# Performance work log

Hardware: AMD Instinct MI355X
Metric: run time of the kernel (lower is better)

The kernel has to match this reference:

```python
import jax, jax.numpy as jnp
import numpy as np

EDGE = 32          # ImageEdge
KPOOL = 16         # pool_kernel_size = ImageEdge // 2
POOLED = 17        # 1 + ImageEdge - pool_kernel_size
NH = 12            # num_attention_heads
HD = 64            # head_dim
HID = 768          # hidden_size
SR = 2             # ScaleRatio


def setup_inputs() -> dict:
    key = jax.random.key(0)
    k1, k2, k3, k4 = jax.random.split(key, 4)
    B, Q = 8, 2048
    return {
        "image_hidden_states": jax.random.normal(k1, (B, EDGE * EDGE, HID), jnp.float32),
        "text_hidden_states": jax.random.normal(k2, (B, Q, HID), jnp.float32),
        "W_in": jax.random.normal(k3, (HID, HID), jnp.float32) * 0.02,   # input_proj (no bias)
        "W_up": jax.random.normal(k4, (HD, HD * SR * SR), jnp.float32) * 0.02,  # up_proj (no bias)
    }


def reference(image_hidden_states, text_hidden_states, W_in, W_up):
    img, txt = image_hidden_states, text_hidden_states
    B, S, HSZ = img.shape            # S = 1024
    Q = txt.shape[1]
    residual = img

    # cross-attention: text queries attend over image keys
    q = txt.reshape(B, Q, NH, HD).transpose(0, 2, 1, 3)   # [B,H,Q,D]
    k = img.reshape(B, S, NH, HD).transpose(0, 2, 1, 3)   # [B,H,S,D]
    attn = jnp.einsum('bhqd,bhkd->bhqk', q, k) / jnp.sqrt(jnp.float32(HD))
    attn = jax.nn.softmax(attn, axis=-1)                  # [B,H,Q,S]
    # dropout is identity in eval mode

    # pooled attention saliency map
    image_attn = attn.sum(axis=2).reshape(B, NH, EDGE, EDGE)
    pooled = jax.lax.reduce_window(
        image_attn, 0.0, jax.lax.add,
        window_dimensions=(1, 1, KPOOL, KPOOL),
        window_strides=(1, 1, 1, 1), padding='VALID') / (KPOOL * KPOOL)   # [B,H,17,17]
    idx = jnp.argmax(pooled.reshape(B, NH, -1), axis=-1)  # [B,H]
    row = (idx // POOLED).reshape(-1)
    col = (idx % POOLED).reshape(-1)

    # gather the argmax-selected 16x16 region per (batch, head)
    states = img.reshape(B, S, NH, HD).transpose(0, 2, 1, 3)
    states = states.reshape(B * NH, EDGE, EDGE, HD)
    slice_one = lambda s, r, c: jax.lax.dynamic_slice(s, (r, c, 0), (KPOOL, KPOOL, HD))
    region = jax.vmap(slice_one)(states, row, col)        # [B*H,16,16,D]

    # pixel-shuffle upsample back to 32x32
    up = region @ W_up                                    # [B*H,16,16,4*D]
    up = up.reshape(B, NH, KPOOL, KPOOL, SR, SR, HD)
    up = up.transpose(0, 1, 2, 4, 3, 5, 6)                # [B,H,16,2,16,2,D]
    up = up.reshape(B, NH, EDGE * EDGE, HD)
    out = up.transpose(0, 2, 1, 3).reshape(B, EDGE * EDGE, HSZ)

    # dense proj + gelu + residual
    out = jax.nn.gelu(out @ W_in, approximate=False)
    return residual + out
```

## Files before the change

### kernel.cpp

```cpp
#include <hip/hip_runtime.h>
#include <cstdint>
#include <cstddef>

#define BB    8
#define NH    12
#define BH    96
#define SS    1024
#define QQ    2048
#define DD    64
#define HID   768
#define EDGE  32
#define KPOOL 16
#define POOLED 17

typedef short bf16x8 __attribute__((ext_vector_type(8)));
typedef _Float16 f16x8 __attribute__((ext_vector_type(8)));
typedef float f32x4  __attribute__((ext_vector_type(4)));

#define MFMA16B(a, b, c) __builtin_amdgcn_mfma_f32_16x16x32_bf16((a), (b), (c), 0, 0, 0)
#define MFMA16H(a, b, c) __builtin_amdgcn_mfma_f32_16x16x32_f16((a), (b), (c), 0, 0, 0)

#define QSCALE 0.18033688011112042f

#if __has_builtin(__builtin_amdgcn_exp2f)
#define EXP2(x) __builtin_amdgcn_exp2f(x)
#else
#define EXP2(x) exp2f(x)
#endif

__device__ __forceinline__ short f2bf(float x) {
    unsigned u = __builtin_bit_cast(unsigned, x);
    u = u + 0x7fffu + ((u >> 16) & 1u);
    return (short)(u >> 16);
}
__device__ __forceinline__ short f2h(float x) {
    _Float16 h = (_Float16)x;
    return __builtin_bit_cast(short, h);
}
__device__ __forceinline__ f16x8 ash(bf16x8 v) {
    return __builtin_bit_cast(f16x8, v);
}

__device__ __forceinline__ size_t fragaddr(int row, int k) {
    return ((size_t)(row >> 4) * 24 + (k >> 5)) * 512 + ((k >> 3) & 3) * 128
         + (row & 15) * 8 + (k & 7);
}


__global__ __launch_bounds__(256) void k_castq(const float* __restrict__ txt,
                                               short* __restrict__ Qs) {
    int i = blockIdx.x * 256 + threadIdx.x;
    int quad = i & 3, kh = (i >> 2) & 1;
    int row = i >> 3;
    int c = row & 15, g = row >> 4;
    int q = row & 2047, bh = row >> 11;
    int b = bh / NH, h = bh - b * NH;
    const float* sp = txt + ((size_t)b * QQ + q) * HID + h * DD + kh * 32 + quad * 8;
    bf16x8 vh, vl;
#pragma unroll
    for (int j = 0; j < 8; j++) {
        float x = sp[j] * QSCALE;
        _Float16 hi = (_Float16)x;
        vh[j] = __builtin_bit_cast(short, hi);
        vl[j] = f2h(x - (float)hi);
    }
    short* dp = Qs + (size_t)g * 2048 + kh * 512 + quad * 128 + c * 8;
    *(bf16x8*)dp = vh;
    *(bf16x8*)(dp + 1024) = vl;
}

__global__ __launch_bounds__(256) void k_castk(const float* __restrict__ img,
                                               short* __restrict__ Ks) {
    int i = blockIdx.x * 256 + threadIdx.x;
    int quad = i & 3, kh = (i >> 2) & 1;
    int row = i >> 3;
    int c = row & 15, g = row >> 4;
    int s = row & 1023, bh = row >> 10;
    int b = bh / NH, h = bh - b * NH;
    const float* sp = img + ((size_t)b * SS + s) * HID + h * DD + kh * 32 + quad * 8;
    bf16x8 vh;
#pragma unroll
    for (int j = 0; j < 8; j++) {
        float x = sp[j];
        _Float16 hi = (_Float16)x;
        vh[j] = __builtin_bit_cast(short, hi);
    }
    short* dp = Ks + (size_t)g * 2048 + kh * 512 + quad * 128 + c * 8;
    *(bf16x8*)dp = vh;
}

__global__ __launch_bounds__(256) void k_castw(const float* __restrict__ W,
                                               const float* __restrict__ Wup,
                                               short* __restrict__ Wt,
                                               short* __restrict__ Wupb) {
    if (blockIdx.x == 144) {
        for (int i = threadIdx.x; i < 16384; i += 256) {
            int k = i >> 8, n = i & 255;
            int addr = (n >> 4) * 1024 + (k >> 5) * 512 + ((k >> 3) & 3) * 128
                     + (n & 15) * 8 + (k & 7);
            Wupb[addr] = f2bf(Wup[k * 256 + n]);
        }
        return;
    }
    __shared__ float T[64][65];
    int bx = blockIdx.x % 12, by = blockIdx.x / 12;
    for (int i = threadIdx.x; i < 4096; i += 256) {
        int r = i >> 6, cc = i & 63;
        T[r][cc] = W[(size_t)(by * 64 + r) * HID + bx * 64 + cc];
    }
    __syncthreads();
    for (int i = threadIdx.x; i < 4096; i += 256) {
        int r = i >> 6, cc = i & 63;
        int n = bx * 64 + r, k = by * 64 + cc;
        Wt[fragaddr(n, k)] = f2bf(T[cc][r]);
    }
}

__global__ __launch_bounds__(256, 2) void k_lsum(const short* __restrict__ Qs,
                                                 const short* __restrict__ Ks,
                                                 float* __restrict__ Lsum) {
    __shared__ short Kt[2][4096];
    int bh = blockIdx.x % BH;
    int qblk = blockIdx.x / BH;
    int tid = threadIdx.x;
    int w = tid >> 6, lane = tid & 63;
    int quad = lane >> 4, c = lane & 15;

    f16x8 a0[4], a1[4];
    const short* qbase = Qs + (size_t)bh * QQ * 128;
#pragma unroll
    for (int t = 0; t < 4; t++) {
        const short* ap = qbase + (size_t)(qblk * 16 + w * 4 + t) * 2048 + lane * 8;
        a0[t] = ash(*(const bf16x8*)(ap));
        a1[t] = ash(*(const bf16x8*)(ap + 512));
    }
    f32x4 lacc[4];
#pragma unroll
    for (int t = 0; t < 4; t++) lacc[t] = (f32x4){0.f, 0.f, 0.f, 0.f};

    const short* kbase = Ks + (size_t)bh * SS * 128;
    int sg = tid >> 7, so = tid & 127;
    bf16x8 st[2];
#pragma unroll
    for (int j = 0; j < 2; j++)
        st[j] = *(const bf16x8*)(kbase + (size_t)(j * 2 + sg) * 2048 + so * 8);

    for (int t1 = 0; t1 < 16; t1++) {
        int buf = t1 & 1;
#pragma unroll
        for (int j = 0; j < 2; j++)
            *(bf16x8*)(&Kt[buf][j * 2048 + tid * 8]) = st[j];
        if (t1 + 1 < 16) {
#pragma unroll
            for (int j = 0; j < 2; j++)
                st[j] = *(const bf16x8*)(kbase + (size_t)((t1 + 1) * 4 + j * 2 + sg) * 2048 + so * 8);
        }
        __syncthreads();
#pragma unroll
        for (int g = 0; g < 4; g++) {
            const short* kp = &Kt[buf][g * 1024 + lane * 8];
            f16x8 kb0 = ash(*(const bf16x8*)(kp));
            f16x8 kb1 = ash(*(const bf16x8*)(kp + 512));
#pragma unroll
            for (int t = 0; t < 4; t++) {
                f32x4 acc = (f32x4){0.f, 0.f, 0.f, 0.f};
                acc = MFMA16H(a0[t], kb0, acc);
                acc = MFMA16H(a1[t], kb1, acc);
#pragma unroll
                for (int r = 0; r < 4; r++) lacc[t][r] += EXP2(acc[r]);
            }
        }
    }
#pragma unroll
    for (int t = 0; t < 4; t++) {
#pragma unroll
        for (int r = 0; r < 4; r++) {
            float v = lacc[t][r];
            v += __shfl_xor(v, 1);
            v += __shfl_xor(v, 2);
            v += __shfl_xor(v, 4);
            v += __shfl_xor(v, 8);
            if (c == 0)
                Lsum[(size_t)bh * QQ + qblk * 256 + w * 64 + t * 16 + quad * 4 + r] = v;
        }
    }
}

__global__ __launch_bounds__(256, 2) void k_attnacc(const short* __restrict__ Qs,
                                                    const short* __restrict__ Ks,
                                                    const float* __restrict__ Lsum,
                                                    float* __restrict__ iattn) {
    __shared__ short Qt[2][8192];
    int bh = blockIdx.x % BH;
    int rem = blockIdx.x / BH;
    int sblk = rem >> 1, qh = rem & 1;
    int tid = threadIdx.x;
    int w = tid >> 6, lane = tid & 63;
    int quad = lane >> 4, c = lane & 15;

    f16x8 ah0[4], ah1[4];
    const short* kbase = Ks + (size_t)bh * SS * 128;
#pragma unroll
    for (int t = 0; t < 4; t++) {
        const short* ap = kbase + (size_t)(sblk * 16 + w * 4 + t) * 2048 + lane * 8;
        ah0[t] = ash(*(const bf16x8*)(ap));
        ah1[t] = ash(*(const bf16x8*)(ap + 512));
    }
    f32x4 racc[4];
#pragma unroll
    for (int t = 0; t < 4; t++) racc[t] = (f32x4){0.f, 0.f, 0.f, 0.f};

    const short* qbase = Qs + ((size_t)bh * QQ + qh * 1024) * 128;
    const float* lbase = Lsum + (size_t)bh * QQ + qh * 1024;

    bf16x8 st[4];
#pragma unroll
    for (int j = 0; j < 4; j++)
        st[j] = *(const bf16x8*)(qbase + (size_t)j * 2048 + tid * 8);

    for (int t2 = 0; t2 < 16; t2++) {
        int buf = t2 & 1;
#pragma unroll
        for (int j = 0; j < 4; j++)
            *(bf16x8*)(&Qt[buf][j * 2048 + tid * 8]) = st[j];
        if (t2 + 1 < 16) {
#pragma unroll
            for (int j = 0; j < 4; j++)
                st[j] = *(const bf16x8*)(qbase + (size_t)(t2 + 1) * 8192 + j * 2048 + tid * 8);
        }
        __syncthreads();
        float rl[4];
#pragma unroll
        for (int g = 0; g < 4; g++)
            rl[g] = __builtin_amdgcn_rcpf(lbase[t2 * 64 + g * 16 + c]);
#pragma unroll
        for (int g = 0; g < 4; g++) {
            const short* qp = &Qt[buf][g * 2048 + lane * 8];
            f16x8 qb0 = ash(*(const bf16x8*)(qp));
            f16x8 qb1 = ash(*(const bf16x8*)(qp + 512));
            f16x8 qb2 = ash(*(const bf16x8*)(qp + 1024));
            f16x8 qb3 = ash(*(const bf16x8*)(qp + 1536));
#pragma unroll
            for (int t = 0; t < 4; t++) {
                f32x4 acc = (f32x4){0.f, 0.f, 0.f, 0.f};
                acc = MFMA16H(ah0[t], qb0, acc);
                acc = MFMA16H(ah1[t], qb1, acc);
                acc = MFMA16H(ah0[t], qb2, acc);
                acc = MFMA16H(ah1[t], qb3, acc);
#pragma unroll
                for (int r = 0; r < 4; r++)
                    racc[t][r] = fmaf(EXP2(acc[r]), rl[g], racc[t][r]);
            }
        }
    }
#pragma unroll
    for (int t = 0; t < 4; t++) {
#pragma unroll
        for (int r = 0; r < 4; r++) {
            float v = racc[t][r];
            v += __shfl_xor(v, 1);
            v += __shfl_xor(v, 2);
            v += __shfl_xor(v, 4);
            v += __shfl_xor(v, 8);
            if (c == 0)
                atomicAdd(&iattn[(size_t)bh * SS + sblk * 256 + w * 64 + t * 16 + quad * 4 + r], v);
        }
    }
}

__global__ __launch_bounds__(256, 2) void k_up(const float* __restrict__ img,
                                               const float* __restrict__ iattn,
                                               const short* __restrict__ Wupb,
                                               short* __restrict__ Xb) {
    __shared__ short Reg[16384];
    float* F = (float*)Reg;
    float* Apool = F;
    float* Vp = F + 1024;
    float* bvp = F + 1568;
    int*   bip = (int*)(F + 1824);

    int bh = blockIdx.x >> 2, nq = blockIdx.x & 3;
    int b = bh / NH, h = bh - b * NH;
    int tid = threadIdx.x;
    int w = tid >> 6, lane = tid & 63;
    int quad = lane >> 4, c = lane & 15;

    for (int i = tid; i < 1024; i += 256) Apool[i] = iattn[(size_t)bh * SS + i];
    __syncthreads();
    for (int i = tid; i < POOLED * EDGE; i += 256) {
        int r = i >> 5, cc = i & 31;
        float s = 0.f;
#pragma unroll
        for (int k = 0; k < KPOOL; k++) s += Apool[(r + k) * EDGE + cc];
        Vp[i] = s;
    }
    __syncthreads();
    float best = -1e30f;
    int bidx = 1 << 30;
    for (int i = tid; i < POOLED * POOLED; i += 256) {
        int r = i / POOLED, cc = i - r * POOLED;
        float s = 0.f;
#pragma unroll
        for (int k = 0; k < KPOOL; k++) s += Vp[r * EDGE + cc + k];
        if (s > best || (s == best && i < bidx)) { best = s; bidx = i; }
    }
    bvp[tid] = best;
    bip[tid] = bidx;
    __syncthreads();
    for (int off = 128; off; off >>= 1) {
        if (tid < off) {
            float ov = bvp[tid + off];
            int oi = bip[tid + off];
            if (ov > bvp[tid] || (ov == bvp[tid] && oi < bip[tid])) {
                bvp[tid] = ov;
                bip[tid] = oi;
            }
        }
        __syncthreads();
    }
    int widx = bip[0];
    __syncthreads();
    int r0 = widx / POOLED, c0 = widx - r0 * POOLED;

    for (int p = tid; p < 2048; p += 256) {
        int pos = p >> 3, sub = p & 7;
        int gi = r0 + (pos >> 4), gj = c0 + (pos & 15);
        const float* sp = img + ((size_t)b * SS + gi * EDGE + gj) * HID + h * DD + sub * 8;
        bf16x8 v;
#pragma unroll
        for (int j = 0; j < 8; j++) v[j] = f2bf(sp[j]);
        *(bf16x8*)(&Reg[(pos >> 4) * 1024 + (sub >> 2) * 512 + (sub & 3) * 128 + (pos & 15) * 8]) = v;
    }
    __syncthreads();

    bf16x8 bu[4][2];
#pragma unroll
    for (int u = 0; u < 4; u++) {
#pragma unroll
        for (int kh = 0; kh < 2; kh++)
            bu[u][kh] = *(const bf16x8*)(Wupb + (nq * 4 + u) * 1024 + kh * 512 + lane * 8);
    }

#pragma unroll
    for (int t = 0; t < 4; t++) {
        int g = w * 4 + t;
        bf16x8 a0 = *(const bf16x8*)(&Reg[g * 1024 + lane * 8]);
        bf16x8 a1 = *(const bf16x8*)(&Reg[g * 1024 + 512 + lane * 8]);
#pragma unroll
        for (int u = 0; u < 4; u++) {
            f32x4 acc = (f32x4){0.f, 0.f, 0.f, 0.f};
            acc = MFMA16B(a0, bu[u][0], acc);
            acc = MFMA16B(a1, bu[u][1], acc);
#pragma unroll
            for (int r = 0; r < 4; r++) {
                int pos = g * 16 + quad * 4 + r;
                int oc = nq * 64 + u * 16 + c;
                int i16 = pos >> 4, j16 = pos & 15;
                int a = oc >> 7, bbit = (oc >> 6) & 1, dp = oc & 63;
                int p2 = (2 * i16 + a) * EDGE + (2 * j16 + bbit);
                int row = b * SS + p2, kdim = h * DD + dp;
                Xb[fragaddr(row, kdim)] = f2bf(acc[r]);
            }
        }
    }
}

__global__ __launch_bounds__(256) void k_out(const short* __restrict__ Xb,
                                             const short* __restrict__ Wt,
                                             const float* __restrict__ img,
                                             float* __restrict__ out) {
    __shared__ short At[2][4096];
    __shared__ short Bt[2][2048];
    int mblk = blockIdx.x & 63, nblk = blockIdx.x >> 6;
    int tid = threadIdx.x;
    int w = tid >> 6, lane = tid & 63;
    int quad = lane >> 4, c = lane & 15;
    int gm0 = mblk * 8, gn0 = nblk * 4;
    int m0 = mblk * 128, n0 = nblk * 64;

    int ua1 = tid + 256;
    const short* srcA0 = Xb + ((size_t)(gm0 + (tid >> 6)) * 24) * 512 + (tid & 63) * 8;
    const short* srcA1 = Xb + ((size_t)(gm0 + (ua1 >> 6)) * 24) * 512 + (ua1 & 63) * 8;
    const short* srcB  = Wt + ((size_t)(gn0 + (tid >> 6)) * 24) * 512 + (tid & 63) * 8;

    f32x4 acc[2][4];
#pragma unroll
    for (int t = 0; t < 2; t++)
#pragma unroll
        for (int u = 0; u < 4; u++) acc[t][u] = (f32x4){0.f, 0.f, 0.f, 0.f};

    bf16x8 sa0 = *(const bf16x8*)(srcA0);
    bf16x8 sa1 = *(const bf16x8*)(srcA1);
    bf16x8 sb  = *(const bf16x8*)(srcB);

    for (int kk = 0; kk < 24; kk++) {
        int buf = kk & 1;
        *(bf16x8*)(&At[buf][tid * 8]) = sa0;
        *(bf16x8*)(&At[buf][ua1 * 8]) = sa1;
        *(bf16x8*)(&Bt[buf][tid * 8]) = sb;
        if (kk + 1 < 24) {
            sa0 = *(const bf16x8*)(srcA0 + (kk + 1) * 512);
            sa1 = *(const bf16x8*)(srcA1 + (kk + 1) * 512);
            sb  = *(const bf16x8*)(srcB  + (kk + 1) * 512);
        }
        __syncthreads();
        bf16x8 a0 = *(const bf16x8*)(&At[buf][(2 * w + 0) * 512 + lane * 8]);
        bf16x8 a1 = *(const bf16x8*)(&At[buf][(2 * w + 1) * 512 + lane * 8]);
        bf16x8 b0 = *(const bf16x8*)(&Bt[buf][0 * 512 + lane * 8]);
        bf16x8 b1 = *(const bf16x8*)(&Bt[buf][1 * 512 + lane * 8]);
        bf16x8 b2 = *(const bf16x8*)(&Bt[buf][2 * 512 + lane * 8]);
        bf16x8 b3 = *(const bf16x8*)(&Bt[buf][3 * 512 + lane * 8]);
        acc[0][0] = MFMA16B(a0, b0, acc[0][0]);
        acc[0][1] = MFMA16B(a0, b1, acc[0][1]);
        acc[0][2] = MFMA16B(a0, b2, acc[0][2]);
        acc[0][3] = MFMA16B(a0, b3, acc[0][3]);
        acc[1][0] = MFMA16B(a1, b0, acc[1][0]);
        acc[1][1] = MFMA16B(a1, b1, acc[1][1]);
        acc[1][2] = MFMA16B(a1, b2, acc[1][2]);
        acc[1][3] = MFMA16B(a1, b3, acc[1][3]);
    }

#pragma unroll
    for (int t = 0; t < 2; t++) {
#pragma unroll
        for (int u = 0; u < 4; u++) {
#pragma unroll
            for (int r = 0; r < 4; r++) {
                int row = m0 + w * 32 + t * 16 + quad * 4 + r;
                int col = n0 + u * 16 + c;
                float x = acc[t][u][r];
                float g = 0.5f * x * (1.f + erff(x * 0.70710678118654752f));
                size_t o = (size_t)row * HID + col;
                out[o] = img[o] + g;
            }
        }
    }
}

extern "C" void kernel_launch(void* const* d_in, const int* in_sizes, int n_in,
                              void* d_out, int out_size, void* d_ws, size_t ws_size,
                              hipStream_t stream) {
    const float* img = (const float*)d_in[0];
    const float* txt = (const float*)d_in[1];
    const float* Win = (const float*)d_in[2];
    const float* Wup = (const float*)d_in[3];
    float* out = (float*)d_out;

    char* w = (char*)d_ws;
    short* Qs    = (short*)(w);
    short* Ks    = (short*)(w + 50331648);
    short* Wt    = (short*)(w + 75497472);
    float* Lsum  = (float*)(w + 76677120);
    float* iattn = (float*)(w + 77463552);
    short* Wupb  = (short*)(w + 77856768);
    short* Xb    = (short*)(w);

    k_castq<<<dim3(6144), dim3(256), 0, stream>>>(txt, Qs);
    k_castk<<<dim3(3072), dim3(256), 0, stream>>>(img, Ks);
    k_castw<<<dim3(145), dim3(256), 0, stream>>>(Win, Wup, Wt, Wupb);
    hipMemsetAsync(iattn, 0, (size_t)BH * SS * sizeof(float), stream);
    k_lsum<<<dim3(768), dim3(256), 0, stream>>>(Qs, Ks, Lsum);
    k_attnacc<<<dim3(768), dim3(256), 0, stream>>>(Qs, Ks, Lsum, iattn);
    k_up<<<dim3(384), dim3(256), 0, stream>>>(img, iattn, Wupb, Xb);
    k_out<<<dim3(768), dim3(256), 0, stream>>>(Xb, Wt, img, out);
}
```

Baseline: 272.1 us.

## Fuse softmax row-sum and column-accumulate passes into one attention kernel

Replaces the separate row-sum kernel and attention-accumulate kernel with a single kernel. Each block computes the QK^T tile for 32 query rows against all 1024 keys once, keeps the exponentials in registers, reduces row sums through shared memory and then accumulates normalized column sums into the saliency buffer with atomics. The low-order f16 residual of Q is dropped, so the cast writes half as much data and the QK^T MFMAs are no longer split into a high and a low pass. This trades precision of the attention scores, which feed an argmax, for less compute and memory traffic. It also adds heavy atomic contention, since 64 blocks per head each add to the same 1024 addresses.

After: 263.9 us. -3.0%, faster.

```diff
diff --git a/kernel.cpp b/kernel.cpp
--- a/kernel.cpp
+++ b/kernel.cpp
@@ -33,10 +33,6 @@
     u = u + 0x7fffu + ((u >> 16) & 1u);
     return (short)(u >> 16);
 }
-__device__ __forceinline__ short f2h(float x) {
-    _Float16 h = (_Float16)x;
-    return __builtin_bit_cast(short, h);
-}
 __device__ __forceinline__ f16x8 ash(bf16x8 v) {
     return __builtin_bit_cast(f16x8, v);
 }
@@ -56,17 +52,13 @@
     int q = row & 2047, bh = row >> 11;
     int b = bh / NH, h = bh - b * NH;
     const float* sp = txt + ((size_t)b * QQ + q) * HID + h * DD + kh * 32 + quad * 8;
-    bf16x8 vh, vl;
+    bf16x8 vh;
 #pragma unroll
     for (int j = 0; j < 8; j++) {
-        float x = sp[j] * QSCALE;
-        _Float16 hi = (_Float16)x;
+        _Float16 hi = (_Float16)(sp[j] * QSCALE);
         vh[j] = __builtin_bit_cast(short, hi);
-        vl[j] = f2h(x - (float)hi);
-    }
-    short* dp = Qs + (size_t)g * 2048 + kh * 512 + quad * 128 + c * 8;
-    *(bf16x8*)dp = vh;
-    *(bf16x8*)(dp + 1024) = vl;
+    }
+    *(bf16x8*)(Qs + (size_t)g * 2048 + kh * 512 + quad * 128 + c * 8) = vh;
 }
 
 __global__ __launch_bounds__(256) void k_castk(const float* __restrict__ img,
@@ -81,12 +73,10 @@
     bf16x8 vh;
 #pragma unroll
     for (int j = 0; j < 8; j++) {
-        float x = sp[j];
-        _Float16 hi = (_Float16)x;
+        _Float16 hi = (_Float16)sp[j];
         vh[j] = __builtin_bit_cast(short, hi);
     }
-    short* dp = Ks + (size_t)g * 2048 + kh * 512 + quad * 128 + c * 8;
-    *(bf16x8*)dp = vh;
+    *(bf16x8*)(Ks + (size_t)g * 2048 + kh * 512 + quad * 128 + c * 8) = vh;
 }
 
 __global__ __launch_bounds__(256) void k_castw(const float* __restrict__ W,
@@ -116,156 +106,79 @@
     }
 }
 
-__global__ __launch_bounds__(256, 2) void k_lsum(const short* __restrict__ Qs,
-                                                 const short* __restrict__ Ks,
-                                                 float* __restrict__ Lsum) {
+__global__ __launch_bounds__(512) void k_fused(const short* __restrict__ Qs,
+                                               const short* __restrict__ Ks,
+                                               float* __restrict__ iattn) {
     __shared__ short Kt[2][4096];
-    int bh = blockIdx.x % BH;
-    int qblk = blockIdx.x / BH;
+    __shared__ float iacc[2][1024];
+    __shared__ float Lred[2][4][16];
+
+    int bh = blockIdx.x >> 6, qb = blockIdx.x & 63;
     int tid = threadIdx.x;
     int w = tid >> 6, lane = tid & 63;
+    int qi = w >> 2, si = w & 3;
     int quad = lane >> 4, c = lane & 15;
 
-    f16x8 a0[4], a1[4];
-    const short* qbase = Qs + (size_t)bh * QQ * 128;
-#pragma unroll
-    for (int t = 0; t < 4; t++) {
-        const short* ap = qbase + (size_t)(qblk * 16 + w * 4 + t) * 2048 + lane * 8;
-        a0[t] = ash(*(const bf16x8*)(ap));
-        a1[t] = ash(*(const bf16x8*)(ap + 512));
-    }
-    f32x4 lacc[4];
-#pragma unroll
-    for (int t = 0; t < 4; t++) lacc[t] = (f32x4){0.f, 0.f, 0.f, 0.f};
+    const short* ap = Qs + ((size_t)bh * 128 + qb * 2 + qi) * 2048 + lane * 8;
+    f16x8 a0 = ash(*(const bf16x8*)(ap));
+    f16x8 a1 = ash(*(const bf16x8*)(ap + 512));
 
     const short* kbase = Ks + (size_t)bh * SS * 128;
-    int sg = tid >> 7, so = tid & 127;
-    bf16x8 st[2];
-#pragma unroll
-    for (int j = 0; j < 2; j++)
-        st[j] = *(const bf16x8*)(kbase + (size_t)(j * 2 + sg) * 2048 + so * 8);
-
-    for (int t1 = 0; t1 < 16; t1++) {
-        int buf = t1 & 1;
-#pragma unroll
-        for (int j = 0; j < 2; j++)
-            *(bf16x8*)(&Kt[buf][j * 2048 + tid * 8]) = st[j];
-        if (t1 + 1 < 16) {
-#pragma unroll
-            for (int j = 0; j < 2; j++)
-                st[j] = *(const bf16x8*)(kbase + (size_t)((t1 + 1) * 4 + j * 2 + sg) * 2048 + so * 8);
-        }
+    size_t soff = (size_t)(tid >> 7) * 2048 + (size_t)(tid & 127) * 8;
+
+    f32x4 pt[16];
+    bf16x8 st = *(const bf16x8*)(kbase + soff);
+
+#pragma unroll
+    for (int cc = 0; cc < 16; cc++) {
+        int buf = cc & 1;
+        *(bf16x8*)(&Kt[buf][tid * 8]) = st;
+        if (cc + 1 < 16)
+            st = *(const bf16x8*)(kbase + (size_t)(cc + 1) * 8192 + soff);
         __syncthreads();
-#pragma unroll
-        for (int g = 0; g < 4; g++) {
-            const short* kp = &Kt[buf][g * 1024 + lane * 8];
-            f16x8 kb0 = ash(*(const bf16x8*)(kp));
-            f16x8 kb1 = ash(*(const bf16x8*)(kp + 512));
-#pragma unroll
-            for (int t = 0; t < 4; t++) {
-                f32x4 acc = (f32x4){0.f, 0.f, 0.f, 0.f};
-                acc = MFMA16H(a0[t], kb0, acc);
-                acc = MFMA16H(a1[t], kb1, acc);
-#pragma unroll
-                for (int r = 0; r < 4; r++) lacc[t][r] += EXP2(acc[r]);
-            }
-        }
-    }
-#pragma unroll
-    for (int t = 0; t < 4; t++) {
-#pragma unroll
-        for (int r = 0; r < 4; r++) {
-            float v = lacc[t][r];
-            v += __shfl_xor(v, 1);
-            v += __shfl_xor(v, 2);
-            v += __shfl_xor(v, 4);
-            v += __shfl_xor(v, 8);
-            if (c == 0)
-                Lsum[(size_t)bh * QQ + qblk * 256 + w * 64 + t * 16 + quad * 4 + r] = v;
-        }
-    }
-}
-
-__global__ __launch_bounds__(256, 2) void k_attnacc(const short* __restrict__ Qs,
-                                                    const short* __restrict__ Ks,
-                                                    const float* __restrict__ Lsum,
-                                                    float* __restrict__ iattn) {
-    __shared__ short Qt[2][8192];
-    int bh = blockIdx.x % BH;
-    int rem = blockIdx.x / BH;
-    int sblk = rem >> 1, qh = rem & 1;
-    int tid = threadIdx.x;
-    int w = tid >> 6, lane = tid & 63;
-    int quad = lane >> 4, c = lane & 15;
-
-    f16x8 ah0[4], ah1[4];
-    const short* kbase = Ks + (size_t)bh * SS * 128;
-#pragma unroll
-    for (int t = 0; t < 4; t++) {
-        const short* ap = kbase + (size_t)(sblk * 16 + w * 4 + t) * 2048 + lane * 8;
-        ah0[t] = ash(*(const bf16x8*)(ap));
-        ah1[t] = ash(*(const bf16x8*)(ap + 512));
-    }
-    f32x4 racc[4];
-#pragma unroll
-    for (int t = 0; t < 4; t++) racc[t] = (f32x4){0.f, 0.f, 0.f, 0.f};
-
-    const short* qbase = Qs + ((size_t)bh * QQ + qh * 1024) * 128;
-    const float* lbase = Lsum + (size_t)bh * QQ + qh * 1024;
-
-    bf16x8 st[4];
-#pragma unroll
-    for (int j = 0; j < 4; j++)
-        st[j] = *(const bf16x8*)(qbase + (size_t)j * 2048 + tid * 8);
-
-    for (int t2 = 0; t2 < 16; t2++) {
-        int buf = t2 & 1;
-#pragma unroll
-        for (int j = 0; j < 4; j++)
-            *(bf16x8*)(&Qt[buf][j * 2048 + tid * 8]) = st[j];
-        if (t2 + 1 < 16) {
-#pragma unroll
-            for (int j = 0; j < 4; j++)
-                st[j] = *(const bf16x8*)(qbase + (size_t)(t2 + 1) * 8192 + j * 2048 + tid * 8);
-        }
-        __syncthreads();
-        float rl[4];
-#pragma unroll
-        for (int g = 0; g < 4; g++)
-            rl[g] = __builtin_amdgcn_rcpf(lbase[t2 * 64 + g * 16 + c]);
-#pragma unroll
-        for (int g = 0; g < 4; g++) {
-            const short* qp = &Qt[buf][g * 2048 + lane * 8];
-            f16x8 qb0 = ash(*(const bf16x8*)(qp));
-            f16x8 qb1 = ash(*(const bf16x8*)(qp + 512));
-            f16x8 qb2 = ash(*(const bf16x8*)(qp + 1024));
-            f16x8 qb3 = ash(*(const bf16x8*)(qp + 1536));
-#pragma unroll
-            for (int t = 0; t < 4; t++) {
-                f32x4 acc = (f32x4){0.f, 0.f, 0.f, 0.f};
-                acc = MFMA16H(ah0[t], qb0, acc);
-                acc = MFMA16H(ah1[t], qb1, acc);
-                acc = MFMA16H(ah0[t], qb2, acc);
-                acc = MFMA16H(ah1[t], qb3, acc);
-#pragma unroll
-                for (int r = 0; r < 4; r++)
-                    racc[t][r] = fmaf(EXP2(acc[r]), rl[g], racc[t][r]);
-            }
-        }
-    }
-#pragma unroll
-    for (int t = 0; t < 4; t++) {
-#pragma unroll
-        for (int r = 0; r < 4; r++) {
-            float v = racc[t][r];
-            v += __shfl_xor(v, 1);
-            v += __shfl_xor(v, 2);
-            v += __shfl_xor(v, 4);
-            v += __shfl_xor(v, 8);
-            if (c == 0)
-                atomicAdd(&iattn[(size_t)bh * SS + sblk * 256 + w * 64 + t * 16 + quad * 4 + r], v);
-        }
-    }
+        f16x8 kb0 = ash(*(const bf16x8*)(&Kt[buf][si * 1024 + lane * 8]));
+        f16x8 kb1 = ash(*(const bf16x8*)(&Kt[buf][si * 1024 + 512 + lane * 8]));
+        f32x4 acc = (f32x4){0.f, 0.f, 0.f, 0.f};
+        acc = MFMA16H(a0, kb0, acc);
+        acc = MFMA16H(a1, kb1, acc);
+#pragma unroll
+        for (int r = 0; r < 4; r++) pt[cc][r] = EXP2(acc[r]);
+    }
+
+    float Lp[4], rl[4];
+#pragma unroll
+    for (int r = 0; r < 4; r++) {
+        float v = 0.f;
+#pragma unroll
+        for (int cc = 0; cc < 16; cc++) v += pt[cc][r];
+        v += __shfl_xor(v, 1);
+        v += __shfl_xor(v, 2);
+        v += __shfl_xor(v, 4);
+        v += __shfl_xor(v, 8);
+        Lp[r] = v;
+    }
+    if (c == 0) {
+#pragma unroll
+        for (int r = 0; r < 4; r++) Lred[qi][si][quad * 4 + r] = Lp[r];
+    }
+    __syncthreads();
+#pragma unroll
+    for (int r = 0; r < 4; r++)
+        rl[r] = __builtin_amdgcn_rcpf(
+            Lred[qi][0][quad * 4 + r] + Lred[qi][1][quad * 4 + r] +
+            Lred[qi][2][quad * 4 + r] + Lred[qi][3][quad * 4 + r]);
+
+#pragma unroll
+    for (int cc = 0; cc < 16; cc++) {
+        float v = pt[cc][0] * rl[0] + pt[cc][1] * rl[1]
+                + pt[cc][2] * rl[2] + pt[cc][3] * rl[3];
+        v += __shfl_xor(v, 16);
+        v += __shfl_xor(v, 32);
+        if (lane < 16) iacc[qi][cc * 64 + si * 16 + lane] = v;
+    }
+    __syncthreads();
+    for (int i = tid; i < 1024; i += 512)
+        atomicAdd(&iattn[(size_t)bh * SS + i], iacc[0][i] + iacc[1][i]);
 }
 
 __global__ __launch_bounds__(256, 2) void k_up(const float* __restrict__ img,
@@ -450,7 +363,6 @@
     short* Qs    = (short*)(w);
     short* Ks    = (short*)(w + 50331648);
     short* Wt    = (short*)(w + 75497472);
-    float* Lsum  = (float*)(w + 76677120);
     float* iattn = (float*)(w + 77463552);
     short* Wupb  = (short*)(w + 77856768);
     short* Xb    = (short*)(w);
@@ -459,8 +371,7 @@
     k_castk<<<dim3(3072), dim3(256), 0, stream>>>(img, Ks);
     k_castw<<<dim3(145), dim3(256), 0, stream>>>(Win, Wup, Wt, Wupb);
     hipMemsetAsync(iattn, 0, (size_t)BH * SS * sizeof(float), stream);
-    k_lsum<<<dim3(768), dim3(256), 0, stream>>>(Qs, Ks, Lsum);
-    k_attnacc<<<dim3(768), dim3(256), 0, stream>>>(Qs, Ks, Lsum, iattn);
+    k_fused<<<dim3(6144), dim3(512), 0, stream>>>(Qs, Ks, iattn);
     k_up<<<dim3(384), dim3(256), 0, stream>>>(img, iattn, Wupb, Xb);
     k_out<<<dim3(768), dim3(256), 0, stream>>>(Xb, Wt, img, out);
 }
```
